# Performance work log

Measured on AMD Instinct MI355X. Metric: run time of the kernel, lower is better.

Reference implementation:

```python
import jax, jax.numpy as jnp
import numpy as np

B, T, D, N, K, H = 2, 2048, 2560, 8, 4, 256
G = N // K
WINDOW = 1024
ROPE_BASE = 10000
K_MASK = -2.3819763e+38
EPS = 1e-6


def apply_rope(inputs, positions, base_frequency):
    # inputs: [B, L, n, H]; positions: [B, L]
    head_dim = inputs.shape[-1]
    fraction = 2 * jnp.arange(0, head_dim // 2) / head_dim
    timescale = base_frequency ** fraction
    sinusoid = positions[..., None] / timescale[None, None, :]   # [B, L, H/2]
    sinusoid = sinusoid[..., None, :]                            # [B, L, 1, H/2]
    sin, cos = jnp.sin(sinusoid), jnp.cos(sinusoid)
    first, second = jnp.split(inputs, 2, axis=-1)
    out = jnp.concatenate([first * cos - second * sin,
                           second * cos + first * sin], axis=-1)
    return out.astype(inputs.dtype)


def rms_norm(x, scale):
    # Gemma-style RMSNorm: normalize over last dim, (1 + scale) gain.
    var = jnp.mean(jnp.square(x), axis=-1, keepdims=True)
    return x * jax.lax.rsqrt(var + EPS) * (1.0 + scale)


def setup_inputs() -> dict:
    key = jax.random.key(0)
    ks = jax.random.split(key, 5)
    x = jax.random.normal(ks[0], (B, T, D), jnp.float32)
    positions = jnp.broadcast_to(jnp.arange(T, dtype=jnp.int32), (B, T))
    # Causal sliding-window mask (LOCAL_SLIDING, window=1024), shape [B, 1, T, S].
    qp = jnp.arange(T)[:, None]
    kp = jnp.arange(T)[None, :]
    mask = (kp <= qp) & ((qp - kp) < WINDOW)
    attn_mask = jnp.broadcast_to(mask[None, None], (B, 1, T, T))
    q_w = jax.random.normal(ks[1], (N, D, H), jnp.float32) * 0.02
    kv_w = jax.random.normal(ks[2], (2, K, D, H), jnp.float32) * 0.02
    q_scale = jnp.zeros((H,), jnp.float32)
    k_scale = jnp.zeros((H,), jnp.float32)
    out_w = jax.random.normal(ks[3], (N, H, D), jnp.float32) * 0.02
    return {"x": x, "q_w": q_w, "kv_w": kv_w, "q_scale": q_scale,
            "k_scale": k_scale, "out_w": out_w,
            "positions": positions, "attn_mask": attn_mask}


def reference(x, q_w, kv_w, q_scale, k_scale, out_w, positions, attn_mask):
    dtype = x.dtype
    # GQA projections (num_kv_heads != num_heads branch)
    q = jnp.einsum('BTD,NDH->BTNH', x, q_w)          # [B,T,N,H]
    k = jnp.einsum('BSD,KDH->BSKH', x, kv_w[0])      # [B,S,K,H]
    v = jnp.einsum('BSD,KDH->BSKH', x, kv_w[1])      # [B,S,K,H]
    # QK-RMSNorm (GQA branch only)
    q = rms_norm(q, q_scale)
    k = rms_norm(k, k_scale)
    # RoPE + query scaling
    q = apply_rope(q, positions, ROPE_BASE)
    q = q * (H ** -0.5)
    k = apply_rope(k, positions, ROPE_BASE)
    # Grouped attention logits: [B,T,K,G,S] -> [B,T,N,S]
    qg = q.reshape(B, T, K, G, H)
    logits = jnp.einsum('BTKGH,BSKH->BTKGS', qg, k)
    logits = logits.reshape(B, T, N, T)
    # Mask + softmax (mask [B,1,T,S] -> [B,T,1,S])
    bmask = jnp.expand_dims(attn_mask.squeeze(axis=1), axis=2)
    masked = jnp.where(bmask, logits, K_MASK)
    probs = jax.nn.softmax(masked, axis=-1).astype(dtype)
    # Weighted values with grouped kv heads
    pg = probs.reshape(B, T, K, G, T)
    enc = jnp.einsum('BTKGS,BSKH->BTKGH', pg, v).reshape(B, T, N, H)
    out = jnp.einsum('BTNH,NHD->BTD', enc, out_w)
    return out
```

## Files before the change

kernel.cpp:

```cpp
#include <hip/hip_runtime.h>
#include <cstdint>

#define TB 2048
#define DIM 2560
#define NQ 8
#define NKV 4
#define HDIM 256
#define WIN 1024
#define KMASK -2.3819763e+38f

using f32x4 = __attribute__((ext_vector_type(4))) float;
using s16x8 = __attribute__((ext_vector_type(8))) short;
using u16x4 = __attribute__((ext_vector_type(4))) unsigned short;

__device__ __forceinline__ unsigned short f2bf(float f) {
  uint32_t x = __builtin_bit_cast(uint32_t, f);
  x += 0x7FFFu + ((x >> 16) & 1u);
  return (unsigned short)(x >> 16);
}

__global__ __launch_bounds__(256) void k_packw1(const float* __restrict__ q_w,
                                                const float* __restrict__ kv_w,
                                                unsigned short* __restrict__ W1) {
  __shared__ float tile[32][33];
  const int hd = blockIdx.z;
  const float* src = (hd < 8) ? (q_w + (size_t)hd * DIM * HDIM)
                              : (kv_w + (size_t)(hd - 8) * DIM * HDIM);
  unsigned short* dst = W1 + (size_t)hd * HDIM * DIM;
  const int c0 = blockIdx.x * 32, r0 = blockIdx.y * 32;
  const int tx = threadIdx.x & 31, ty = threadIdx.x >> 5;
#pragma unroll
  for (int i = 0; i < 32; i += 8)
    tile[ty + i][tx] = src[(size_t)(r0 + ty + i) * HDIM + c0 + tx];
  __syncthreads();
#pragma unroll
  for (int i = 0; i < 32; i += 8)
    dst[(size_t)(c0 + ty + i) * DIM + r0 + tx] = f2bf(tile[tx][ty + i]);
}

__global__ __launch_bounds__(256) void k_tconv(const float* __restrict__ src,
                                               unsigned short* __restrict__ dst,
                                               int R, int C) {
  __shared__ float tile[32][33];
  const int c0 = blockIdx.x * 32, r0 = blockIdx.y * 32;
  const int tx = threadIdx.x & 31, ty = threadIdx.x >> 5;
#pragma unroll
  for (int i = 0; i < 32; i += 8)
    tile[ty + i][tx] = src[(size_t)(r0 + ty + i) * C + c0 + tx];
  __syncthreads();
#pragma unroll
  for (int i = 0; i < 32; i += 8)
    dst[(size_t)(c0 + ty + i) * R + r0 + tx] = f2bf(tile[tx][ty + i]);
}

__global__ __launch_bounds__(256) void k_cvt(const float* __restrict__ src,
                                             unsigned short* __restrict__ dst, int n4) {
  int i = blockIdx.x * 256 + threadIdx.x;
  if (i < n4) {
    f32x4 v = *(const f32x4*)&src[(size_t)i * 4];
    u16x4 o;
#pragma unroll
    for (int j = 0; j < 4; ++j) o[j] = f2bf(v[j]);
    *(u16x4*)&dst[(size_t)i * 4] = o;
  }
}

__global__ __launch_bounds__(512, 2) void k_gemm(const unsigned short* __restrict__ A,
                                                 const unsigned short* __restrict__ Bw,
                                                 float* __restrict__ Cc,
                                                 int Nc, int Kd, int nxl) {
  __shared__ unsigned short shA[2][256 * 64];
  __shared__ unsigned short shB[2][256 * 64];
  const int tid = threadIdx.x, w = tid >> 6, l = tid & 63;
  const int xcd = blockIdx.x & 7, loc = blockIdx.x >> 3;
  const int m0 = ((xcd >> 1) * 4 + loc / nxl) * 256;
  const int n0 = ((xcd & 1) * nxl + loc % nxl) * 256;

  const int srow = l >> 3;
  const int sw_colb = (((l & 7) ^ srow) << 4);
  const int wrow = w * 8;
  const int NT = Kd >> 6;

#define GSTAGE(buf, t)                                                                      \
  {                                                                                         \
    const size_t kt = (size_t)(t) << 6;                                                     \
    _Pragma("unroll") for (int r = 0; r < 4; ++r) {                                         \
      const char* src = (const char*)A + ((size_t)(m0 + r * 64 + wrow + srow) * Kd + kt) * 2 + sw_colb; \
      __builtin_amdgcn_global_load_lds(                                                     \
          (__attribute__((address_space(1))) void*)src,                                     \
          (__attribute__((address_space(3))) void*)((char*)&shA[buf][0] + r * 8192 + w * 1024), \
          16, 0, 0);                                                                        \
    }                                                                                       \
    _Pragma("unroll") for (int r = 0; r < 4; ++r) {                                         \
      const char* src = (const char*)Bw + ((size_t)(n0 + r * 64 + wrow + srow) * Kd + kt) * 2 + sw_colb; \
      __builtin_amdgcn_global_load_lds(                                                     \
          (__attribute__((address_space(1))) void*)src,                                     \
          (__attribute__((address_space(3))) void*)((char*)&shB[buf][0] + r * 8192 + w * 1024), \
          16, 0, 0);                                                                        \
    }                                                                                       \
  }

  const int wm = w >> 2, wn = w & 3;
  const int lr = l & 15, lg = l >> 4;
  f32x4 acc[8][4] = {};

  GSTAGE(0, 0);

  for (int t = 0; t < NT; ++t) {
    const int buf = t & 1;
    if (t + 1 < NT) {
      GSTAGE(buf ^ 1, t + 1);
      asm volatile("s_waitcnt vmcnt(8)" ::: "memory");
    } else {
      asm volatile("s_waitcnt vmcnt(0)" ::: "memory");
    }
    __builtin_amdgcn_s_barrier();

    const char* sa = (const char*)&shA[buf][0];
    const char* sb = (const char*)&shB[buf][0];
#pragma unroll
    for (int kk = 0; kk < 2; ++kk) {
      const int cb = kk * 64 + lg * 16;
      const int cbx = cb ^ ((lr & 7) << 4);
      s16x8 af[8], bfr[4];
#pragma unroll
      for (int mi = 0; mi < 8; ++mi)
        af[mi] = *(const s16x8*)(sa + (wm * 128 + mi * 16 + lr) * 128 + cbx);
#pragma unroll
      for (int ni = 0; ni < 4; ++ni)
        bfr[ni] = *(const s16x8*)(sb + (wn * 64 + ni * 16 + lr) * 128 + cbx);
      __builtin_amdgcn_s_setprio(1);
#pragma unroll
      for (int mi = 0; mi < 8; ++mi)
#pragma unroll
        for (int ni = 0; ni < 4; ++ni)
          acc[mi][ni] = __builtin_amdgcn_mfma_f32_16x16x32_bf16(af[mi], bfr[ni], acc[mi][ni], 0, 0, 0);
      __builtin_amdgcn_s_setprio(0);
    }
    __builtin_amdgcn_s_barrier();
  }
#undef GSTAGE

#pragma unroll
  for (int mi = 0; mi < 8; ++mi)
#pragma unroll
    for (int ni = 0; ni < 4; ++ni) {
      size_t base = (size_t)(m0 + wm * 128 + mi * 16 + lg * 4) * Nc + (n0 + wn * 64 + ni * 16 + lr);
#pragma unroll
      for (int i = 0; i < 4; ++i)
        Cc[base + (size_t)i * Nc] = acc[mi][ni][i];
    }
}

__global__ __launch_bounds__(256) void k_normrope(const float* __restrict__ Y,
                                                  const float* __restrict__ qsc,
                                                  const float* __restrict__ ksc,
                                                  const int* __restrict__ pos,
                                                  unsigned short* __restrict__ Q,
                                                  unsigned short* __restrict__ Kb) {
  __shared__ float s_sin[128], s_cos[128];
  const int bt = blockIdx.x;
  const int b = bt >> 11, t = bt & (TB - 1);
  const int tid = threadIdx.x;
  float p = (float)pos[bt];
  if (tid < 128) {
    float fr = (float)tid * (1.0f / 128.0f);
    float inv_ts = __expf(fr * -9.210340371976184f);
    float ang = p * inv_ts;
    float sv, cv;
    sincosf(ang, &sv, &cv);
    s_sin[tid] = sv;
    s_cos[tid] = cv;
  }
  __syncthreads();
  const int w = tid >> 6, l = tid & 63;
  const int jj0 = (l & 31) * 4;
  for (int sidx = w; sidx < 12; sidx += 4) {
    const float* src = Y + (size_t)bt * 4096 + sidx * 256;
    f32x4 v = *(const f32x4*)&src[l * 4];
    float ss = v[0] * v[0] + v[1] * v[1] + v[2] * v[2] + v[3] * v[3];
#pragma unroll
    for (int d = 1; d < 64; d <<= 1) ss += __shfl_xor(ss, d);
    float rs = rsqrtf(ss * (1.0f / 256.0f) + 1e-6f);
    const float* scp = (sidx < 8) ? qsc : ksc;
    float nv[4], res[4];
#pragma unroll
    for (int j = 0; j < 4; ++j) nv[j] = v[j] * rs * (1.0f + scp[l * 4 + j]);
#pragma unroll
    for (int j = 0; j < 4; ++j) {
      float o = __shfl_xor(nv[j], 32);
      float sn = s_sin[jj0 + j], cs = s_cos[jj0 + j];
      res[j] = (l < 32) ? (nv[j] * cs - o * sn) : (nv[j] * cs + o * sn);
    }
    float qs = (sidx < 8) ? 0.0625f : 1.0f;
    u16x4 ob;
#pragma unroll
    for (int j = 0; j < 4; ++j) ob[j] = f2bf(res[j] * qs);
    if (sidx < 8) {
      size_t di = ((size_t)(b * NQ + sidx) * TB + t) * HDIM + l * 4;
      *(u16x4*)&Q[di] = ob;
    } else {
      size_t di = ((size_t)(b * NKV + (sidx - 8)) * TB + t) * HDIM + l * 4;
      *(u16x4*)&Kb[di] = ob;
    }
  }
}

__global__ __launch_bounds__(256) void k_vtrans(const float* __restrict__ Y,
                                                unsigned short* __restrict__ VT) {
  __shared__ float tile[64][65];
  const int t0 = blockIdx.x * 64, h0 = blockIdx.y * 64;
  const int z = blockIdx.z;
  const int bq = z >> 2, kh = z & 3;
  const int tid = threadIdx.x;
#pragma unroll
  for (int rep = 0; rep < 16; ++rep) {
    int idx = rep * 256 + tid;
    int tr = idx >> 6, hc = idx & 63;
    tile[tr][hc] = Y[(size_t)(bq * TB + t0 + tr) * 4096 + 3072 + kh * 256 + h0 + hc];
  }
  __syncthreads();
#pragma unroll
  for (int rep = 0; rep < 16; ++rep) {
    int idx = rep * 256 + tid;
    int hr = idx >> 6, tc = idx & 63;
    VT[((size_t)z * 256 + h0 + hr) * TB + t0 + tc] = f2bf(tile[tc][hr]);
  }
}

__global__ __launch_bounds__(256, 2) void k_attn(const unsigned short* __restrict__ Q,
                                                 const unsigned short* __restrict__ Kb,
                                                 const unsigned short* __restrict__ VT,
                                                 unsigned short* __restrict__ ENC) {
  __shared__ unsigned short shK[2][32 * 256];
  __shared__ unsigned short shV[2][256 * 32];
  __shared__ unsigned short Pb[4][16 * 40];
  const int tid = threadIdx.x, w = tid >> 6, l = tid & 63;
  const int bn = blockIdx.y;
  const int b = bn >> 3, n = bn & 7, kh = n >> 1;
  const int t0b = blockIdx.x * 64;
  const int t0 = t0b + w * 16;
  const int lr = l & 15, lg = l >> 4;
  const unsigned short* qp = Q + ((size_t)bn * TB + t0) * HDIM;
  const char* kbase = (const char*)(Kb + ((size_t)(b * NKV + kh) * TB) * HDIM);
  const char* vbase = (const char*)(VT + ((size_t)(b * NKV + kh) * HDIM) * TB);

  s16x8 aq[8];
#pragma unroll
  for (int kk = 0; kk < 8; ++kk)
    aq[kk] = *(const s16x8*)&qp[lr * HDIM + kk * 32 + lg * 8];

  f32x4 o[16] = {};
  float mrow[4], lsum[4];
#pragma unroll
  for (int i = 0; i < 4; ++i) { mrow[i] = -__builtin_inff(); lsum[i] = 0.f; }

  int lo = t0b - (WIN - 1);
  if (lo < 0) lo = 0;
  lo &= ~31;
  const int nsteps = (t0b + 32 - lo) / 32 + 1;

  const int k_row = (w << 1) + (l >> 5);
  const int k_colb = (l & 31) * 16;
  const int v_row = (w << 4) + (l >> 2);
  const int v_colb = (l & 3) * 16;
#define STAGE(buf, s0)                                                                       \
  {                                                                                          \
    _Pragma("unroll") for (int r = 0; r < 4; ++r) {                                          \
      int row = r * 8 + k_row;                                                               \
      int scol = k_colb ^ ((row & 7) << 4);                                                  \
      const char* src = kbase + (size_t)((s0) + row) * 512 + scol;                           \
      __builtin_amdgcn_global_load_lds(                                                      \
          (__attribute__((address_space(1))) void*)src,                                      \
          (__attribute__((address_space(3))) void*)((char*)&shK[buf][0] + r * 4096 + w * 1024), \
          16, 0, 0);                                                                         \
    }                                                                                        \
    _Pragma("unroll") for (int r = 0; r < 4; ++r) {                                          \
      int row = r * 64 + v_row;                                                              \
      const char* src = vbase + (size_t)row * (TB * 2) + (size_t)(s0) * 2 + v_colb;          \
      __builtin_amdgcn_global_load_lds(                                                      \
          (__attribute__((address_space(1))) void*)src,                                      \
          (__attribute__((address_space(3))) void*)((char*)&shV[buf][0] + r * 4096 + w * 1024), \
          16, 0, 0);                                                                         \
    }                                                                                        \
  }

  STAGE(0, lo);

  for (int step = 0; step < nsteps; ++step) {
    const int s0 = lo + step * 32;
    const int buf = step & 1;
    if (step + 1 < nsteps) {
      STAGE(buf ^ 1, s0 + 32);
      asm volatile("s_waitcnt vmcnt(8)" ::: "memory");
    } else {
      asm volatile("s_waitcnt vmcnt(0)" ::: "memory");
    }
    __builtin_amdgcn_s_barrier();

    const bool active = (s0 <= t0 + 15) && (s0 + 31 >= t0 - (WIN - 1));
    if (active) {
      f32x4 sacc[2] = {};
      const char* kt = (const char*)&shK[buf][0];
      const int swz = (lr & 7) << 4;
#pragma unroll
      for (int cb = 0; cb < 2; ++cb) {
        const int rb = (cb * 16 + lr) * 512;
        s16x8 bk[8];
#pragma unroll
        for (int kk = 0; kk < 8; ++kk)
          bk[kk] = *(const s16x8*)(kt + rb + ((kk * 64 + lg * 16) ^ swz));
        __builtin_amdgcn_s_setprio(1);
#pragma unroll
        for (int kk = 0; kk < 8; ++kk)
          sacc[cb] = __builtin_amdgcn_mfma_f32_16x16x32_bf16(aq[kk], bk[kk], sacc[cb], 0, 0, 0);
        __builtin_amdgcn_s_setprio(0);
      }
      float svA_[4], svB_[4];
      const bool nomask = (s0 + 31 <= t0) && (s0 >= t0 - (WIN - 16));
      if (nomask) {
#pragma unroll
        for (int i = 0; i < 4; ++i) { svA_[i] = sacc[0][i]; svB_[i] = sacc[1][i]; }
      } else {
#pragma unroll
        for (int i = 0; i < 4; ++i) {
          int trow = t0 + lg * 4 + i;
          int sA = s0 + lr, sB = s0 + 16 + lr;
          svA_[i] = ((sA <= trow) && (trow - sA < WIN)) ? sacc[0][i] : KMASK;
          svB_[i] = ((sB <= trow) && (trow - sB < WIN)) ? sacc[1][i] : KMASK;
        }
      }
      bool ok = true;
#pragma unroll
      for (int i = 0; i < 4; ++i)
        ok = ok && (svA_[i] <= mrow[i] + 8.f) && (svB_[i] <= mrow[i] + 8.f);
      if (!__all(ok)) {
        float r_[4];
#pragma unroll
        for (int i = 0; i < 4; ++i) {
          float mx = fmaxf(svA_[i], svB_[i]);
#pragma unroll
          for (int d = 1; d < 16; d <<= 1) mx = fmaxf(mx, __shfl_xor(mx, d));
          float mnew = fmaxf(mrow[i], mx);
          r_[i] = __expf(mrow[i] - mnew);
          lsum[i] *= r_[i];
          mrow[i] = mnew;
        }
#pragma unroll
        for (int hb = 0; hb < 16; ++hb)
#pragma unroll
          for (int i = 0; i < 4; ++i) o[hb][i] *= r_[i];
      }
#pragma unroll
      for (int i = 0; i < 4; ++i) {
        float pa = __expf(svA_[i] - mrow[i]);
        float pb = __expf(svB_[i] - mrow[i]);
        lsum[i] += pa + pb;
        int row = lg * 4 + i;
        Pb[w][row * 40 + lr] = f2bf(pa);
        Pb[w][row * 40 + 16 + lr] = f2bf(pb);
      }
      asm volatile("s_waitcnt lgkmcnt(0)" ::: "memory");
      s16x8 pfrag = *(const s16x8*)&Pb[w][lr * 40 + lg * 8];
      const char* vt = (const char*)&shV[buf][0];
      s16x8 vb[16];
#pragma unroll
      for (int hb = 0; hb < 16; ++hb)
        vb[hb] = *(const s16x8*)(vt + (hb * 16 + lr) * 64 + lg * 16);
      __builtin_amdgcn_s_setprio(1);
#pragma unroll
      for (int hb = 0; hb < 16; ++hb)
        o[hb] = __builtin_amdgcn_mfma_f32_16x16x32_bf16(pfrag, vb[hb], o[hb], 0, 0, 0);
      __builtin_amdgcn_s_setprio(0);
    }
    __builtin_amdgcn_s_barrier();
  }
#undef STAGE

#pragma unroll
  for (int i = 0; i < 4; ++i) {
    float s = lsum[i];
#pragma unroll
    for (int d = 1; d < 16; d <<= 1) s += __shfl_xor(s, d);
    lsum[i] = s;
  }
#pragma unroll
  for (int i = 0; i < 4; ++i) {
    int trow = t0 + lg * 4 + i;
    float inv = 1.0f / lsum[i];
    size_t rb = (size_t)(b * TB + trow) * 2048 + n * HDIM;
#pragma unroll
    for (int hb = 0; hb < 16; ++hb)
      ENC[rb + hb * 16 + lr] = f2bf(o[hb][i] * inv);
  }
}

extern "C" void kernel_launch(void* const* d_in, const int* in_sizes, int n_in,
                              void* d_out, int out_size, void* d_ws, size_t ws_size,
                              hipStream_t stream) {
  (void)in_sizes; (void)n_in; (void)out_size; (void)ws_size;
  const float* x = (const float*)d_in[0];
  const float* q_w = (const float*)d_in[1];
  const float* kv_w = (const float*)d_in[2];
  const float* qsc = (const float*)d_in[3];
  const float* ksc = (const float*)d_in[4];
  const float* out_w = (const float*)d_in[5];
  const int* pos = (const int*)d_in[6];
  float* out = (float*)d_out;

  char* ws = (char*)d_ws;
  unsigned short* W1 = (unsigned short*)(ws);
  unsigned short* W3 = (unsigned short*)(ws + 20971520);
  unsigned short* XB = (unsigned short*)(ws + 31457280);
  float* Y = (float*)(ws + 52428800);
  unsigned short* KB = (unsigned short*)(ws + 119537664);
  unsigned short* VT = (unsigned short*)(ws + 127926272);
  unsigned short* Qb = XB;
  unsigned short* ENC = (unsigned short*)(ws + 52428800);

  k_packw1<<<dim3(8, 80, 16), 256, 0, stream>>>(q_w, kv_w, W1);
  k_tconv<<<dim3(80, 64), 256, 0, stream>>>(out_w, W3, 2048, DIM);
  k_cvt<<<dim3(10240), 256, 0, stream>>>(x, XB, 2621440);
  k_gemm<<<dim3(256), 512, 0, stream>>>(XB, W1, Y, 4096, DIM, 8);
  k_normrope<<<dim3(4096), 256, 0, stream>>>(Y, qsc, ksc, pos, Qb, KB);
  k_vtrans<<<dim3(32, 4, 8), 256, 0, stream>>>(Y, VT);
  k_attn<<<dim3(32, 16), 256, 0, stream>>>(Qb, KB, VT, ENC);
  k_gemm<<<dim3(160), 512, 0, stream>>>(ENC, W3, out, DIM, 2048, 5);
}
```

Baseline: 272.4 us.

## Interleave GEMM tile prefetch with four-phase MFMA clusters per K-step

Restructures the bf16 GEMM main loop into four phases per 64-wide K tile. Each phase loads half of the A fragments (and B fragments where needed) from LDS, issues a quarter of the next tile's global-to-LDS loads, and runs a 16-MFMA cluster between barriers. The goal is to spread global load issue and LDS reads across the compute instead of bunching them at the start of each tile, and to hold fewer fragment registers at once. In exchange it adds more barriers per iteration and a full vmcnt(0) wait at the end of each step, which may limit how far loads run ahead.

```diff
diff --git a/kernel.cpp b/kernel.cpp
--- a/kernel.cpp
+++ b/kernel.cpp
@@ -81,65 +81,113 @@
   const int wrow = w * 8;
   const int NT = Kd >> 6;
 
-#define GSTAGE(buf, t)                                                                      \
-  {                                                                                         \
-    const size_t kt = (size_t)(t) << 6;                                                     \
-    _Pragma("unroll") for (int r = 0; r < 4; ++r) {                                         \
-      const char* src = (const char*)A + ((size_t)(m0 + r * 64 + wrow + srow) * Kd + kt) * 2 + sw_colb; \
-      __builtin_amdgcn_global_load_lds(                                                     \
-          (__attribute__((address_space(1))) void*)src,                                     \
-          (__attribute__((address_space(3))) void*)((char*)&shA[buf][0] + r * 8192 + w * 1024), \
-          16, 0, 0);                                                                        \
-    }                                                                                       \
-    _Pragma("unroll") for (int r = 0; r < 4; ++r) {                                         \
-      const char* src = (const char*)Bw + ((size_t)(n0 + r * 64 + wrow + srow) * Kd + kt) * 2 + sw_colb; \
-      __builtin_amdgcn_global_load_lds(                                                     \
-          (__attribute__((address_space(1))) void*)src,                                     \
-          (__attribute__((address_space(3))) void*)((char*)&shB[buf][0] + r * 8192 + w * 1024), \
-          16, 0, 0);                                                                        \
-    }                                                                                       \
+#define STG_A(buf, t, r)                                                                     \
+  {                                                                                          \
+    const char* src_ = (const char*)A +                                                      \
+        ((size_t)(m0 + (r) * 64 + wrow + srow) * Kd + ((size_t)(t) << 6)) * 2 + sw_colb;     \
+    __builtin_amdgcn_global_load_lds(                                                        \
+        (__attribute__((address_space(1))) void*)src_,                                       \
+        (__attribute__((address_space(3))) void*)((char*)&shA[buf][0] + (r) * 8192 + w * 1024), \
+        16, 0, 0);                                                                           \
+  }
+#define STG_B(buf, t, r)                                                                     \
+  {                                                                                          \
+    const char* src_ = (const char*)Bw +                                                     \
+        ((size_t)(n0 + (r) * 64 + wrow + srow) * Kd + ((size_t)(t) << 6)) * 2 + sw_colb;     \
+    __builtin_amdgcn_global_load_lds(                                                        \
+        (__attribute__((address_space(1))) void*)src_,                                       \
+        (__attribute__((address_space(3))) void*)((char*)&shB[buf][0] + (r) * 8192 + w * 1024), \
+        16, 0, 0);                                                                           \
   }
 
   const int wm = w >> 2, wn = w & 3;
   const int lr = l & 15, lg = l >> 4;
+  const int rswz = (lr & 7) << 4;
+  const int c0x = (lg * 16) ^ rswz;
+  const int c1x = (64 + lg * 16) ^ rswz;
   f32x4 acc[8][4] = {};
 
-  GSTAGE(0, 0);
+#pragma unroll
+  for (int r = 0; r < 4; ++r) { STG_A(0, 0, r); STG_B(0, 0, r); }
+  asm volatile("s_waitcnt vmcnt(0)" ::: "memory");
+  __builtin_amdgcn_s_barrier();
 
   for (int t = 0; t < NT; ++t) {
     const int buf = t & 1;
-    if (t + 1 < NT) {
-      GSTAGE(buf ^ 1, t + 1);
-      asm volatile("s_waitcnt vmcnt(8)" ::: "memory");
-    } else {
-      asm volatile("s_waitcnt vmcnt(0)" ::: "memory");
-    }
-    __builtin_amdgcn_s_barrier();
-
+    const bool pf = (t + 1 < NT);
     const char* sa = (const char*)&shA[buf][0];
     const char* sb = (const char*)&shB[buf][0];
-#pragma unroll
-    for (int kk = 0; kk < 2; ++kk) {
-      const int cb = kk * 64 + lg * 16;
-      const int cbx = cb ^ ((lr & 7) << 4);
-      s16x8 af[8], bfr[4];
-#pragma unroll
-      for (int mi = 0; mi < 8; ++mi)
-        af[mi] = *(const s16x8*)(sa + (wm * 128 + mi * 16 + lr) * 128 + cbx);
+    s16x8 af[4], bf0[4], bf1[4];
+
+#pragma unroll
+    for (int mi = 0; mi < 4; ++mi)
+      af[mi] = *(const s16x8*)(sa + (wm * 128 + mi * 16 + lr) * 128 + c0x);
+#pragma unroll
+    for (int ni = 0; ni < 4; ++ni)
+      bf0[ni] = *(const s16x8*)(sb + (wn * 64 + ni * 16 + lr) * 128 + c0x);
+    if (pf) { STG_A(buf ^ 1, t + 1, 0); STG_A(buf ^ 1, t + 1, 1); }
+    __builtin_amdgcn_s_barrier();
+    asm volatile("s_waitcnt lgkmcnt(0)" ::: "memory");
+    __builtin_amdgcn_s_setprio(1);
+#pragma unroll
+    for (int mi = 0; mi < 4; ++mi)
 #pragma unroll
       for (int ni = 0; ni < 4; ++ni)
-        bfr[ni] = *(const s16x8*)(sb + (wn * 64 + ni * 16 + lr) * 128 + cbx);
-      __builtin_amdgcn_s_setprio(1);
-#pragma unroll
-      for (int mi = 0; mi < 8; ++mi)
-#pragma unroll
-        for (int ni = 0; ni < 4; ++ni)
-          acc[mi][ni] = __builtin_amdgcn_mfma_f32_16x16x32_bf16(af[mi], bfr[ni], acc[mi][ni], 0, 0, 0);
-      __builtin_amdgcn_s_setprio(0);
-    }
-    __builtin_amdgcn_s_barrier();
-  }
-#undef GSTAGE
+        acc[mi][ni] = __builtin_amdgcn_mfma_f32_16x16x32_bf16(af[mi], bf0[ni], acc[mi][ni], 0, 0, 0);
+    __builtin_amdgcn_s_setprio(0);
+    __builtin_amdgcn_s_barrier();
+
+#pragma unroll
+    for (int mi = 0; mi < 4; ++mi)
+      af[mi] = *(const s16x8*)(sa + (wm * 128 + (4 + mi) * 16 + lr) * 128 + c0x);
+    if (pf) { STG_A(buf ^ 1, t + 1, 2); STG_A(buf ^ 1, t + 1, 3); }
+    __builtin_amdgcn_s_barrier();
+    asm volatile("s_waitcnt lgkmcnt(0)" ::: "memory");
+    __builtin_amdgcn_s_setprio(1);
+#pragma unroll
+    for (int mi = 0; mi < 4; ++mi)
+#pragma unroll
+      for (int ni = 0; ni < 4; ++ni)
+        acc[4 + mi][ni] = __builtin_amdgcn_mfma_f32_16x16x32_bf16(af[mi], bf0[ni], acc[4 + mi][ni], 0, 0, 0);
+    __builtin_amdgcn_s_setprio(0);
+    __builtin_amdgcn_s_barrier();
+
+#pragma unroll
+    for (int mi = 0; mi < 4; ++mi)
+      af[mi] = *(const s16x8*)(sa + (wm * 128 + mi * 16 + lr) * 128 + c1x);
+#pragma unroll
+    for (int ni = 0; ni < 4; ++ni)
+      bf1[ni] = *(const s16x8*)(sb + (wn * 64 + ni * 16 + lr) * 128 + c1x);
+    if (pf) { STG_B(buf ^ 1, t + 1, 0); STG_B(buf ^ 1, t + 1, 1); }
+    __builtin_amdgcn_s_barrier();
+    asm volatile("s_waitcnt lgkmcnt(0)" ::: "memory");
+    __builtin_amdgcn_s_setprio(1);
+#pragma unroll
+    for (int mi = 0; mi < 4; ++mi)
+#pragma unroll
+      for (int ni = 0; ni < 4; ++ni)
+        acc[mi][ni] = __builtin_amdgcn_mfma_f32_16x16x32_bf16(af[mi], bf1[ni], acc[mi][ni], 0, 0, 0);
+    __builtin_amdgcn_s_setprio(0);
+    __builtin_amdgcn_s_barrier();
+
+#pragma unroll
+    for (int mi = 0; mi < 4; ++mi)
+      af[mi] = *(const s16x8*)(sa + (wm * 128 + (4 + mi) * 16 + lr) * 128 + c1x);
+    if (pf) { STG_B(buf ^ 1, t + 1, 2); STG_B(buf ^ 1, t + 1, 3); }
+    __builtin_amdgcn_s_barrier();
+    asm volatile("s_waitcnt lgkmcnt(0)" ::: "memory");
+    __builtin_amdgcn_s_setprio(1);
+#pragma unroll
+    for (int mi = 0; mi < 4; ++mi)
+#pragma unroll
+      for (int ni = 0; ni < 4; ++ni)
+        acc[4 + mi][ni] = __builtin_amdgcn_mfma_f32_16x16x32_bf16(af[mi], bf1[ni], acc[4 + mi][ni], 0, 0, 0);
+    __builtin_amdgcn_s_setprio(0);
+    asm volatile("s_waitcnt vmcnt(0)" ::: "memory");
+    __builtin_amdgcn_s_barrier();
+  }
+#undef STG_A
+#undef STG_B
 
 #pragma unroll
   for (int mi = 0; mi < 8; ++mi)
```

New measurement: 260.8 us. 1.04x faster.
